# Kernel tuning notes

Hardware: AMD Instinct MI355X
Metric: run time of the kernel (lower is better)

## Reference

```python
import jax, jax.numpy as jnp
import numpy as np

NUM_CENTROIDS = 8192
COMMITMENT = 0.25


def setup_inputs() -> dict:
    key = jax.random.key(0)
    k1, k2 = jax.random.split(key)
    B, T, D, K = 16, 2048, 512, NUM_CENTROIDS
    inputs = jax.random.normal(k1, (B, T, D), dtype=jnp.float32)
    # kaiming_normal_ on [K, D]: std = sqrt(2 / fan_in) with fan_in = D
    codebook = jax.random.normal(k2, (K, D), dtype=jnp.float32) * jnp.sqrt(2.0 / D)
    return {"inputs": inputs, "codebook": codebook, "train": 0}


def reference(inputs, codebook, train):
    D = inputs.shape[-1]
    K = codebook.shape[0]
    flat = inputs.reshape(-1, D)  # [N, D]

    distances = (
        jnp.sum(flat * flat, axis=1, keepdims=True)
        - 2.0 * (flat @ codebook.T)
        + jnp.sum(codebook * codebook, axis=1)[None, :]
    )
    nn_idx = jnp.argmin(distances, axis=1)  # [N]

    # one_hot @ codebook == gather (same math, no [N, K] one-hot materialized)
    quantized = codebook[nn_idx]  # [N, D]

    # VQ loss (codebook term) + commitment term
    quant_loss = jnp.square(quantized - jax.lax.stop_gradient(flat))
    quant_loss = quant_loss + COMMITMENT * jnp.square(
        jax.lax.stop_gradient(quantized) - flat
    )
    quantization_loss = quant_loss.reshape(inputs.shape)

    quantized = quantized.reshape(inputs.shape)
    # straight-through estimator
    quantized_out = inputs + jax.lax.stop_gradient(quantized - inputs)

    nn_idx = nn_idx.reshape(inputs.shape[:-1])[None, ...]  # [1, B, T]
    codebook_values = jax.lax.stop_gradient(codebook)[None, ...]  # [1, K, D]
    counts = jnp.ones((K,), dtype=jnp.float32)  # train=False: EMA counter untouched (init ones)

    return quantized_out, quantization_loss, nn_idx, codebook_values, counts
```

## Files before the change

kernel.cpp:

```cpp
#include <hip/hip_runtime.h>

#define NROWS 32768
#define DDIM  512
#define KCENT 8192

#define O_LOSS 16777216
#define O_IDX  33554432
#define O_CBV  33587200
#define O_CNT  37781504
#define O_PBLK 8388608

typedef float f32x4 __attribute__((ext_vector_type(4)));
typedef _Float16 f16x8 __attribute__((ext_vector_type(8)));

__global__ __launch_bounds__(256) void vq_cvt_swz8(
    const float* __restrict__ src, char* __restrict__ dst)
{
    const int gid = blockIdx.x * 256 + threadIdx.x;
    const int r = gid >> 6, w = gid & 63, dk = w >> 3, u = w & 7;
    const float4* p = (const float4*)(src + (size_t)r * DDIM + (dk*8 + (u ^ (r & 7))) * 8);
    float4 a = p[0], b = p[1];
    f16x8 h;
    h[0]=(_Float16)a.x; h[1]=(_Float16)a.y; h[2]=(_Float16)a.z; h[3]=(_Float16)a.w;
    h[4]=(_Float16)b.x; h[5]=(_Float16)b.y; h[6]=(_Float16)b.z; h[7]=(_Float16)b.w;
    *(f16x8*)(dst + (size_t)gid * 16) = h;
}

__global__ __launch_bounds__(256) void vq_cnorm_kernel(
    const float* __restrict__ CB, float* __restrict__ cnorm, float* __restrict__ counts)
{
    const int wid  = threadIdx.x >> 6;
    const int lane = threadIdx.x & 63;
    const int cid  = blockIdx.x * 4 + wid;
    const float4* p = (const float4*)(CB + (size_t)cid * DDIM + lane * 8);
    float4 a = p[0], b = p[1];
    double s = (double)a.x*a.x + (double)a.y*a.y + (double)a.z*a.z + (double)a.w*a.w
             + (double)b.x*b.x + (double)b.y*b.y + (double)b.z*b.z + (double)b.w*b.w;
    #pragma unroll
    for (int off = 32; off > 0; off >>= 1) s += __shfl_down(s, off);
    if (lane == 0) { cnorm[cid] = (float)s; counts[cid] = 1.0f; }
}

__device__ __forceinline__ void t2_merge(float b1, int bi1, float b2, int bi2,
                                         float& a1, int& ai1, float& a2, int& ai2)
{
    if (b1 < a1 || (b1 == a1 && bi1 < ai1)) {
        float o1 = a1; int oi1 = ai1;
        a1 = b1; ai1 = bi1;
        if (b2 < o1 || (b2 == o1 && bi2 < oi1)) { a2 = b2; ai2 = bi2; }
        else                                    { a2 = o1; ai2 = oi1; }
    } else {
        if (b1 < a2 || (b1 == a2 && bi1 < ai2)) { a2 = b1; ai2 = bi1; }
    }
}

__device__ __forceinline__ void gl16(const char* g, const char* l)
{
    __builtin_amdgcn_global_load_lds(
        (const __attribute__((address_space(1))) void*)g,
        (__attribute__((address_space(3))) void*)l, 16, 0, 0);
}

__global__ __launch_bounds__(512, 4) void vq_gemm_kernel(
    const char* __restrict__ Xf, const char* __restrict__ Cf,
    const float* __restrict__ cnorm, float4* __restrict__ pblk)
{
    __shared__ __align__(16) char lds[32768];

    const int bid = blockIdx.x;
    const int xcd = bid & 7;
    const int idx = bid >> 3;
    const int cb  = xcd * 8 + (idx & 7);
    const int rb  = idx >> 3;

    const int t    = threadIdx.x;
    const int lane = t & 63;
    const int wid  = t >> 6;
    const int wr   = wid >> 2;
    const int wc   = wid & 3;
    const int l15  = lane & 15;
    const int lg   = lane >> 4;

    const int r0 = t >> 3,        u0 = t & 7;
    const int r1 = (t + 512) >> 3, u1 = (t + 512) & 7;
    const size_t a0 = (size_t)(rb*128 + r0)*1024 + u0*16;
    const size_t a1 = (size_t)(rb*128 + r1)*1024 + u1*16;
    const size_t b0 = (size_t)(cb*128 + r0)*1024 + u0*16;
    const size_t b1 = (size_t)(cb*128 + r1)*1024 + u1*16;
    char* la0 = &lds[t*16];
    char* la1 = &lds[(t+512)*16];
    char* lb0 = &lds[16384 + t*16];
    char* lb1 = &lds[16384 + (t+512)*16];

    f32x4 z4 = {0.f, 0.f, 0.f, 0.f};
    f32x4 a00=z4, a01=z4, a10=z4, a11=z4, a20=z4, a21=z4, a30=z4, a31=z4;

    for (int dk = 0; dk < 8; ++dk) {
        __syncthreads();
        gl16(Xf + a0 + dk*128, la0);
        gl16(Xf + a1 + dk*128, la1);
        gl16(Cf + b0 + dk*128, lb0);
        gl16(Cf + b1 + dk*128, lb1);
        __syncthreads();

        #pragma unroll
        for (int ks = 0; ks < 2; ++ks) {
            const int ku = ks*4 + lg;
            const int rA0 = wr*64 +  0 + l15, rA1 = wr*64 + 16 + l15;
            const int rA2 = wr*64 + 32 + l15, rA3 = wr*64 + 48 + l15;
            const int rB0 = wc*32 +  0 + l15, rB1 = wc*32 + 16 + l15;
            f16x8 A0 = *(const f16x8*)(&lds[rA0*128 + ((ku ^ (rA0 & 7)) * 16)]);
            f16x8 A1 = *(const f16x8*)(&lds[rA1*128 + ((ku ^ (rA1 & 7)) * 16)]);
            f16x8 A2 = *(const f16x8*)(&lds[rA2*128 + ((ku ^ (rA2 & 7)) * 16)]);
            f16x8 A3 = *(const f16x8*)(&lds[rA3*128 + ((ku ^ (rA3 & 7)) * 16)]);
            f16x8 B0 = *(const f16x8*)(&lds[16384 + rB0*128 + ((ku ^ (rB0 & 7)) * 16)]);
            f16x8 B1 = *(const f16x8*)(&lds[16384 + rB1*128 + ((ku ^ (rB1 & 7)) * 16)]);
            a00 = __builtin_amdgcn_mfma_f32_16x16x32_f16(A0, B0, a00, 0, 0, 0);
            a01 = __builtin_amdgcn_mfma_f32_16x16x32_f16(A0, B1, a01, 0, 0, 0);
            a10 = __builtin_amdgcn_mfma_f32_16x16x32_f16(A1, B0, a10, 0, 0, 0);
            a11 = __builtin_amdgcn_mfma_f32_16x16x32_f16(A1, B1, a11, 0, 0, 0);
            a20 = __builtin_amdgcn_mfma_f32_16x16x32_f16(A2, B0, a20, 0, 0, 0);
            a21 = __builtin_amdgcn_mfma_f32_16x16x32_f16(A2, B1, a21, 0, 0, 0);
            a30 = __builtin_amdgcn_mfma_f32_16x16x32_f16(A3, B0, a30, 0, 0, 0);
            a31 = __builtin_amdgcn_mfma_f32_16x16x32_f16(A3, B1, a31, 0, 0, 0);
        }
    }
    __syncthreads();

    const int colbase = cb*128 + wc*32;
    const float cn0 = cnorm[colbase + l15];
    const float cn1 = cnorm[colbase + 16 + l15];
    const int   c0  = colbase + l15;
    const int   c1  = colbase + 16 + l15;
    float4* redq = (float4*)&lds[0];

    #define T2EPI(M, AC0, AC1)                                                   \
        _Pragma("unroll")                                                        \
        for (int j = 0; j < 4; ++j) {                                            \
            float s0 = fmaf(-2.0f, AC0[j], cn0);                                 \
            float s1 = fmaf(-2.0f, AC1[j], cn1);                                 \
            float v1, v2; int i1, i2;                                            \
            if (s0 <= s1) { v1=s0; i1=c0; v2=s1; i2=c1; }                        \
            else          { v1=s1; i1=c1; v2=s0; i2=c0; }                        \
            _Pragma("unroll")                                                    \
            for (int off = 1; off <= 8; off <<= 1) {                             \
                float e1 = __shfl_xor(v1, off), e2 = __shfl_xor(v2, off);        \
                int  f1 = __shfl_xor(i1, off),  f2 = __shfl_xor(i2, off);        \
                t2_merge(e1, f1, e2, f2, v1, i1, v2, i2);                        \
            }                                                                    \
            if (l15 == 0) {                                                      \
                float4 w; w.x = v1; w.y = __int_as_float(i1);                    \
                w.z = v2; w.w = __int_as_float(i2);                              \
                redq[(wr*64 + M*16 + lg*4 + j)*4 + wc] = w;                      \
            }                                                                    \
        }

    T2EPI(0, a00, a01)
    T2EPI(1, a10, a11)
    T2EPI(2, a20, a21)
    T2EPI(3, a30, a31)
    #undef T2EPI

    __syncthreads();
    if (t < 128) {
        float4 e0 = redq[t*4 + 0], e1 = redq[t*4 + 1];
        float4 e2 = redq[t*4 + 2], e3 = redq[t*4 + 3];
        float v1 = e0.x, v2 = e0.z;
        int   i1 = __float_as_int(e0.y), i2 = __float_as_int(e0.w);
        t2_merge(e1.x, __float_as_int(e1.y), e1.z, __float_as_int(e1.w), v1, i1, v2, i2);
        t2_merge(e2.x, __float_as_int(e2.y), e2.z, __float_as_int(e2.w), v1, i1, v2, i2);
        t2_merge(e3.x, __float_as_int(e3.y), e3.z, __float_as_int(e3.w), v1, i1, v2, i2);
        float4 w; w.x = v1; w.y = __int_as_float(i1); w.z = v2; w.w = __int_as_float(i2);
        pblk[((size_t)(rb*128 + t))*64 + cb] = w;
    }
}

__global__ __launch_bounds__(256) void vq_merge_kernel(
    const float4* __restrict__ pblk, int* __restrict__ pmini2)
{
    const int wid  = threadIdx.x >> 6;
    const int lane = threadIdx.x & 63;
    const int row  = blockIdx.x * 4 + wid;
    float4 e = pblk[(size_t)row*64 + lane];
    float v1 = e.x, v2 = e.z;
    int   i1 = __float_as_int(e.y), i2 = __float_as_int(e.w);
    #pragma unroll
    for (int off = 1; off < 64; off <<= 1) {
        float b1 = __shfl_xor(v1, off), b2 = __shfl_xor(v2, off);
        int  c1 = __shfl_xor(i1, off),  c2 = __shfl_xor(i2, off);
        t2_merge(b1, c1, b2, c2, v1, i1, v2, i2);
    }
    if (lane == 0) { pmini2[row*2 + 0] = i1; pmini2[row*2 + 1] = i2; }
}

__global__ __launch_bounds__(256) void vq_resolve_out(
    const float* __restrict__ X, const float* __restrict__ CB,
    const int* __restrict__ pmini2, float* __restrict__ out)
{
    const int wid  = threadIdx.x >> 6;
    const int lane = threadIdx.x & 63;
    const int row  = blockIdx.x * 4 + wid;
    const int i0 = pmini2[row*2 + 0], i1 = pmini2[row*2 + 1];

    const float4* xp = (const float4*)(X + (size_t)row * DDIM + lane * 8);
    float4 xa = xp[0], xb = xp[1];
    const float4* p0 = (const float4*)(CB + (size_t)i0 * DDIM + lane * 8);
    float4 c0a = p0[0], c0b = p0[1];
    const float4* p1 = (const float4*)(CB + (size_t)i1 * DDIM + lane * 8);
    float4 c1a = p1[0], c1b = p1[1];

    double d0 = 0.0, d1 = 0.0, e;
    e = (double)xa.x - c0a.x; d0 += e*e;  e = (double)xa.y - c0a.y; d0 += e*e;
    e = (double)xa.z - c0a.z; d0 += e*e;  e = (double)xa.w - c0a.w; d0 += e*e;
    e = (double)xb.x - c0b.x; d0 += e*e;  e = (double)xb.y - c0b.y; d0 += e*e;
    e = (double)xb.z - c0b.z; d0 += e*e;  e = (double)xb.w - c0b.w; d0 += e*e;
    e = (double)xa.x - c1a.x; d1 += e*e;  e = (double)xa.y - c1a.y; d1 += e*e;
    e = (double)xa.z - c1a.z; d1 += e*e;  e = (double)xa.w - c1a.w; d1 += e*e;
    e = (double)xb.x - c1b.x; d1 += e*e;  e = (double)xb.y - c1b.y; d1 += e*e;
    e = (double)xb.z - c1b.z; d1 += e*e;  e = (double)xb.w - c1b.w; d1 += e*e;
    #pragma unroll
    for (int off = 1; off < 64; off <<= 1) {
        d0 += __shfl_xor(d0, off);
        d1 += __shfl_xor(d1, off);
    }

    const bool w1 = (d1 < d0) || (d1 == d0 && i1 < i0);
    const int idxw = w1 ? i1 : i0;
    float4 qa, qb;
    qa.x = w1 ? c1a.x : c0a.x;  qa.y = w1 ? c1a.y : c0a.y;
    qa.z = w1 ? c1a.z : c0a.z;  qa.w = w1 ? c1a.w : c0a.w;
    qb.x = w1 ? c1b.x : c0b.x;  qb.y = w1 ? c1b.y : c0b.y;
    qb.z = w1 ? c1b.z : c0b.z;  qb.w = w1 ? c1b.w : c0b.w;

    float4 qoa, loa, qob, lob;
    float d, s;
    d = qa.x - xa.x; qoa.x = xa.x + d; s = d*d; loa.x = s + 0.25f*s;
    d = qa.y - xa.y; qoa.y = xa.y + d; s = d*d; loa.y = s + 0.25f*s;
    d = qa.z - xa.z; qoa.z = xa.z + d; s = d*d; loa.z = s + 0.25f*s;
    d = qa.w - xa.w; qoa.w = xa.w + d; s = d*d; loa.w = s + 0.25f*s;
    d = qb.x - xb.x; qob.x = xb.x + d; s = d*d; lob.x = s + 0.25f*s;
    d = qb.y - xb.y; qob.y = xb.y + d; s = d*d; lob.y = s + 0.25f*s;
    d = qb.z - xb.z; qob.z = xb.z + d; s = d*d; lob.z = s + 0.25f*s;
    d = qb.w - xb.w; qob.w = xb.w + d; s = d*d; lob.w = s + 0.25f*s;

    ((float4*)out)[(size_t)row*128 + lane*2 + 0] = qoa;
    ((float4*)out)[(size_t)row*128 + lane*2 + 1] = qob;
    ((float4*)(out + O_LOSS))[(size_t)row*128 + lane*2 + 0] = loa;
    ((float4*)(out + O_LOSS))[(size_t)row*128 + lane*2 + 1] = lob;
    if (lane == 0) out[O_IDX + row] = (float)idxw;
}

extern "C" void kernel_launch(void* const* d_in, const int* in_sizes, int n_in,
                              void* d_out, int out_size, void* d_ws, size_t ws_size,
                              hipStream_t stream)
{
    const float* X  = (const float*)d_in[0];
    const float* CB = (const float*)d_in[1];
    float* out = (float*)d_out;

    char*   XsB  = (char*)out;
    float4* pblk = (float4*)(out + O_PBLK);
    char*   CBsB = (char*)(out + O_LOSS);

    float* cnorm  = (float*)d_ws;
    int*   pmini2 = (int*)(cnorm + KCENT);

    vq_cvt_swz8<<<(NROWS*64)/256, 256, 0, stream>>>(X, XsB);
    vq_cvt_swz8<<<(KCENT*64)/256, 256, 0, stream>>>(CB, CBsB);
    vq_cnorm_kernel<<<KCENT/4, 256, 0, stream>>>(CB, cnorm, out + O_CNT);
    vq_gemm_kernel<<<(NROWS/128)*(KCENT/128), 512, 0, stream>>>(XsB, CBsB, cnorm, pblk);
    vq_merge_kernel<<<NROWS/4, 256, 0, stream>>>(pblk, pmini2);
    vq_resolve_out<<<NROWS/4, 256, 0, stream>>>(X, CB, pmini2, out);
    hipMemcpyAsync(out + O_CBV, CB, (size_t)KCENT * DDIM * sizeof(float),
                   hipMemcpyDeviceToDevice, stream);
}
```

Measured before the change: 791.0 us.

## Double-buffer LDS tiles with async global_load_lds prefetch of next K step

Doubles the shared-memory tile buffer and issues the global-to-LDS loads for the next K slice before computing on the current one, waiting with a partial vmcnt counter and a raw s_barrier. This overlaps memory latency with MFMA work instead of fully serialising load and compute each step. LDS use doubles to 64KB per block, which may limit occupancy at the launch bound of 4 blocks, and the hand-written waitcnt/barrier sequence depends on the compiler not reordering LDS reads.

```diff
diff --git a/kernel.cpp b/kernel.cpp
--- a/kernel.cpp
+++ b/kernel.cpp
@@ -65,7 +65,7 @@
     const char* __restrict__ Xf, const char* __restrict__ Cf,
     const float* __restrict__ cnorm, float4* __restrict__ pblk)
 {
-    __shared__ __align__(16) char lds[32768];
+    __shared__ __align__(16) char lds[2][32768];
 
     const int bid = blockIdx.x;
     const int xcd = bid & 7;
@@ -81,40 +81,47 @@
     const int l15  = lane & 15;
     const int lg   = lane >> 4;
 
-    const int r0 = t >> 3,        u0 = t & 7;
+    const int r0 = t >> 3,         u0 = t & 7;
     const int r1 = (t + 512) >> 3, u1 = (t + 512) & 7;
     const size_t a0 = (size_t)(rb*128 + r0)*1024 + u0*16;
     const size_t a1 = (size_t)(rb*128 + r1)*1024 + u1*16;
     const size_t b0 = (size_t)(cb*128 + r0)*1024 + u0*16;
     const size_t b1 = (size_t)(cb*128 + r1)*1024 + u1*16;
-    char* la0 = &lds[t*16];
-    char* la1 = &lds[(t+512)*16];
-    char* lb0 = &lds[16384 + t*16];
-    char* lb1 = &lds[16384 + (t+512)*16];
 
     f32x4 z4 = {0.f, 0.f, 0.f, 0.f};
     f32x4 a00=z4, a01=z4, a10=z4, a11=z4, a20=z4, a21=z4, a30=z4, a31=z4;
 
+    #define STAGE(step, buf) do {                                   \
+        const size_t o_ = (size_t)(step) * 128;                     \
+        gl16(Xf + a0 + o_, &lds[buf][t*16]);                        \
+        gl16(Xf + a1 + o_, &lds[buf][(t+512)*16]);                  \
+        gl16(Cf + b0 + o_, &lds[buf][16384 + t*16]);                \
+        gl16(Cf + b1 + o_, &lds[buf][16384 + (t+512)*16]);          \
+    } while (0)
+
+    STAGE(0, 0);
+
+    #pragma unroll
     for (int dk = 0; dk < 8; ++dk) {
-        __syncthreads();
-        gl16(Xf + a0 + dk*128, la0);
-        gl16(Xf + a1 + dk*128, la1);
-        gl16(Cf + b0 + dk*128, lb0);
-        gl16(Cf + b1 + dk*128, lb1);
-        __syncthreads();
-
+        if (dk + 1 < 8) STAGE(dk + 1, (dk + 1) & 1);
+        if (dk + 1 < 8) {
+            asm volatile("s_waitcnt vmcnt(4)\n\ts_barrier" ::: "memory");
+        } else {
+            asm volatile("s_waitcnt vmcnt(0)\n\ts_barrier" ::: "memory");
+        }
+        const char* bb = &lds[dk & 1][0];
         #pragma unroll
         for (int ks = 0; ks < 2; ++ks) {
             const int ku = ks*4 + lg;
             const int rA0 = wr*64 +  0 + l15, rA1 = wr*64 + 16 + l15;
             const int rA2 = wr*64 + 32 + l15, rA3 = wr*64 + 48 + l15;
             const int rB0 = wc*32 +  0 + l15, rB1 = wc*32 + 16 + l15;
-            f16x8 A0 = *(const f16x8*)(&lds[rA0*128 + ((ku ^ (rA0 & 7)) * 16)]);
-            f16x8 A1 = *(const f16x8*)(&lds[rA1*128 + ((ku ^ (rA1 & 7)) * 16)]);
-            f16x8 A2 = *(const f16x8*)(&lds[rA2*128 + ((ku ^ (rA2 & 7)) * 16)]);
-            f16x8 A3 = *(const f16x8*)(&lds[rA3*128 + ((ku ^ (rA3 & 7)) * 16)]);
-            f16x8 B0 = *(const f16x8*)(&lds[16384 + rB0*128 + ((ku ^ (rB0 & 7)) * 16)]);
-            f16x8 B1 = *(const f16x8*)(&lds[16384 + rB1*128 + ((ku ^ (rB1 & 7)) * 16)]);
+            f16x8 A0 = *(const f16x8*)(bb + rA0*128 + ((ku ^ (rA0 & 7)) * 16));
+            f16x8 A1 = *(const f16x8*)(bb + rA1*128 + ((ku ^ (rA1 & 7)) * 16));
+            f16x8 A2 = *(const f16x8*)(bb + rA2*128 + ((ku ^ (rA2 & 7)) * 16));
+            f16x8 A3 = *(const f16x8*)(bb + rA3*128 + ((ku ^ (rA3 & 7)) * 16));
+            f16x8 B0 = *(const f16x8*)(bb + 16384 + rB0*128 + ((ku ^ (rB0 & 7)) * 16));
+            f16x8 B1 = *(const f16x8*)(bb + 16384 + rB1*128 + ((ku ^ (rB1 & 7)) * 16));
             a00 = __builtin_amdgcn_mfma_f32_16x16x32_f16(A0, B0, a00, 0, 0, 0);
             a01 = __builtin_amdgcn_mfma_f32_16x16x32_f16(A0, B1, a01, 0, 0, 0);
             a10 = __builtin_amdgcn_mfma_f32_16x16x32_f16(A1, B0, a10, 0, 0, 0);
@@ -124,7 +131,9 @@
             a30 = __builtin_amdgcn_mfma_f32_16x16x32_f16(A3, B0, a30, 0, 0, 0);
             a31 = __builtin_amdgcn_mfma_f32_16x16x32_f16(A3, B1, a31, 0, 0, 0);
         }
-    }
+        asm volatile("s_barrier" ::: "memory");
+    }
+    #undef STAGE
     __syncthreads();
 
     const int colbase = cb*128 + wc*32;
@@ -132,7 +141,7 @@
     const float cn1 = cnorm[colbase + 16 + l15];
     const int   c0  = colbase + l15;
     const int   c1  = colbase + 16 + l15;
-    float4* redq = (float4*)&lds[0];
+    float4* redq = (float4*)&lds[0][0];
 
     #define T2EPI(M, AC0, AC1)                                                   \
         _Pragma("unroll")                                                        \
```

After: 776.4 us. No clear change (-1.8%).
